# Kernel tuning notes

Measured on AMD Instinct MI355X. Metric: run time of the kernel, lower is better.

The kernel has to match this reference:

```python
import jax, jax.numpy as jnp
import numpy as np

NUM_HEADS = 16


def setup_inputs() -> dict:
    key = jax.random.key(0)
    ks = jax.random.split(key, 10)
    B, S, D = 2, 2048, 1024
    x = jax.random.normal(ks[0], (B, S, D), dtype=jnp.float32)
    mask = jax.random.randint(ks[1], (B, 1, 1, S), 0, 2, dtype=jnp.int32)
    scale = 1.0 / np.sqrt(D)
    wq = jax.random.normal(ks[2], (D, D), dtype=jnp.float32) * scale
    bq = jnp.zeros((D,), dtype=jnp.float32)
    wk = jax.random.normal(ks[3], (D, D), dtype=jnp.float32) * scale
    bk = jnp.zeros((D,), dtype=jnp.float32)
    wv = jax.random.normal(ks[4], (D, D), dtype=jnp.float32) * scale
    bv = jnp.zeros((D,), dtype=jnp.float32)
    wo = jax.random.normal(ks[5], (D, D), dtype=jnp.float32) * scale
    bo = jnp.zeros((D,), dtype=jnp.float32)
    return {"x": x, "mask": mask, "wq": wq, "bq": bq, "wk": wk, "bk": bk,
            "wv": wv, "bv": bv, "wo": wo, "bo": bo}


def reference(x, mask, wq, bq, wk, bk, wv, bv, wo, bo):
    B, S, D = x.shape
    H = NUM_HEADS
    dk = D // H

    def split_heads(t):
        # (B, S, D) -> (B, H, S, dk)
        return t.reshape(B, S, H, dk).transpose(0, 2, 1, 3)

    # PyTorch nn.Linear: y = x @ W^T + b
    q = split_heads(x @ wq.T + bq)
    k = split_heads(x @ wk.T + bk)
    v = split_heads(x @ wv.T + bv)

    # scaled dot-product attention with explicit score matrix (as original)
    logits = jnp.einsum('bhqd,bhkd->bhqk', q, k) / jnp.sqrt(jnp.float32(dk))
    logits = jnp.where(mask == 0, jnp.float32(-1e9), logits)
    attn_weights = jax.nn.softmax(logits, axis=-1)
    # dropout(p=0.1) is identity in eval mode (deterministic reference)
    attn = jnp.einsum('bhqk,bhkd->bhqd', attn_weights, v)

    attn = attn.transpose(0, 2, 1, 3).reshape(B, S, D)
    out = attn @ wo.T + bo
    return out, attn_weights
```

## Files before the change

### kernel.cpp

```cpp
#include <hip/hip_runtime.h>
#include <hip/hip_bf16.h>

#define DEV __device__ __forceinline__

typedef __attribute__((ext_vector_type(8))) __bf16 bf16x8;
typedef __attribute__((ext_vector_type(8))) short s16x8;
typedef __attribute__((ext_vector_type(4))) float f32x4;

DEV f32x4 mfma16(s16x8 a, s16x8 b, f32x4 c){
  return __builtin_amdgcn_mfma_f32_16x16x32_bf16(
      __builtin_bit_cast(bf16x8, a), __builtin_bit_cast(bf16x8, b), c, 0, 0, 0);
}

DEV unsigned short f2bf(float f){
  unsigned int u = __builtin_bit_cast(unsigned int, f);
  u = u + 0x7FFFu + ((u >> 16) & 1u);
  return (unsigned short)(u >> 16);
}

DEV float bf2f(unsigned short u){
  return __builtin_bit_cast(float, ((unsigned int)u) << 16);
}

DEV unsigned long long pack4(float4 v){
  return (unsigned long long)f2bf(v.x) | ((unsigned long long)f2bf(v.y) << 16)
       | ((unsigned long long)f2bf(v.z) << 32) | ((unsigned long long)f2bf(v.w) << 48);
}

DEV unsigned long long pack4f(float a, float b, float c, float d){
  return (unsigned long long)f2bf(a) | ((unsigned long long)f2bf(b) << 16)
       | ((unsigned long long)f2bf(c) << 32) | ((unsigned long long)f2bf(d) << 48);
}

DEV void async16(const void* g, void* l){
  __builtin_amdgcn_global_load_lds(
      (const __attribute__((address_space(1))) unsigned int*)g,
      (__attribute__((address_space(3))) unsigned int*)l, 16, 0, 0);
}

__global__ __launch_bounds__(256) void cvt_kernel(
    const float* __restrict__ x, const float* __restrict__ wq, const float* __restrict__ wk,
    const float* __restrict__ wv, const float* __restrict__ wo,
    const float* __restrict__ bq, const float* __restrict__ bk, const float* __restrict__ bv,
    unsigned long long* __restrict__ xb, unsigned long long* __restrict__ wqkvb,
    unsigned long long* __restrict__ wob, float4* __restrict__ bqkv)
{
  const int i = blockIdx.x * 256 + threadIdx.x;
  const int X4 = 1048576, W4 = 262144;
  if (i < X4){
    xb[i] = pack4(((const float4*)x)[i]);
  } else if (i < X4 + 3*W4){
    int j = i - X4;
    const float* src = (j < W4) ? wq : (j < 2*W4) ? wk : wv;
    int jj = (j < W4) ? j : (j < 2*W4) ? (j - W4) : (j - 2*W4);
    wqkvb[j] = pack4(((const float4*)src)[jj]);
  } else if (i < X4 + 4*W4){
    int j = i - X4 - 3*W4;
    wob[j] = pack4(((const float4*)wo)[j]);
  } else if (i < X4 + 4*W4 + 768){
    int j = i - X4 - 4*W4;
    const float* src = (j < 256) ? bq : (j < 512) ? bk : bv;
    int jj = (j < 256) ? j : (j < 512) ? (j - 256) : (j - 512);
    bqkv[j] = ((const float4*)src)[jj];
  }
}

__global__ __launch_bounds__(256) void gemm_qkv(
    const unsigned short* __restrict__ A,
    const unsigned short* __restrict__ B,
    const float* __restrict__ bias,
    unsigned short* __restrict__ oq,
    unsigned short* __restrict__ okk,
    unsigned short* __restrict__ ovt)
{
  __shared__ __align__(16) char smem[32768];
  char* As = smem;
  char* Bs = smem + 16384;
  const int tid = threadIdx.x;
  const int l = tid & 63, w = tid >> 6, g = l >> 4;

  const int orig = blockIdx.x;
  const int lin = (orig & 7) * 96 + (orig >> 3);
  const int m0 = (lin / 24) * 128, n0 = (lin % 24) * 128;
  const int rowbytes = 2048;

  f32x4 acc[4][4] = {};
  const int wr = w >> 1, wc = w & 1;
  const int wm = wr * 64, wn = wc * 64;

  const int srow = w * 32 + (l >> 3);
  const int scol = (((l & 7) ^ (l >> 3)) << 4);
  const char* Abp = (const char*)A + (size_t)(m0 + srow) * rowbytes + scol;
  const char* Bbp = (const char*)B + (size_t)(n0 + srow) * rowbytes + scol;
  char* Asw = As + w * 4096;
  char* Bsw = Bs + w * 4096;

  int aoff[4][2], boff[4][2];
  for (int mf = 0; mf < 4; ++mf)
    for (int ks = 0; ks < 2; ++ks){
      int ra = wm + mf * 16 + (l & 15);
      aoff[mf][ks] = ra * 128 + ((ks * 64 + g * 16) ^ ((l & 7) << 4));
      int rb = wn + mf * 16 + (l & 15);
      boff[mf][ks] = rb * 128 + ((ks * 64 + g * 16) ^ ((l & 7) << 4));
    }

  for (int kt = 0; kt < 16; ++kt){
    const char* ab = Abp + kt * 128;
    const char* bb = Bbp + kt * 128;
    for (int i = 0; i < 4; ++i){
      async16(ab + (size_t)i * 8 * rowbytes, Asw + i * 1024);
      async16(bb + (size_t)i * 8 * rowbytes, Bsw + i * 1024);
    }
    __syncthreads();
    for (int ks = 0; ks < 2; ++ks){
      s16x8 af[4], bf[4];
      for (int mf = 0; mf < 4; ++mf) af[mf] = *(const s16x8*)(As + aoff[mf][ks]);
      for (int nf = 0; nf < 4; ++nf) bf[nf] = *(const s16x8*)(Bs + boff[nf][ks]);
      for (int mf = 0; mf < 4; ++mf)
        for (int nf = 0; nf < 4; ++nf)
          acc[mf][nf] = mfma16(af[mf], bf[nf], acc[mf][nf]);
    }
    __syncthreads();
  }

  if (n0 >= 2048){
    for (int nf = 0; nf < 4; ++nf){
      int nloc = wn + nf * 16 + (l & 15);
      float bs = bias[n0 + nloc];
      for (int mf = 0; mf < 4; ++mf){
        int mby = (wm + mf * 16 + g * 4) * 2;
        unsigned long long pk = pack4f(acc[mf][nf][0] + bs, acc[mf][nf][1] + bs,
                                       acc[mf][nf][2] + bs, acc[mf][nf][3] + bs);
        *(unsigned long long*)(smem + nloc * 256 + (mby ^ ((nloc & 15) << 4))) = pk;
      }
    }
    __syncthreads();
    int b2 = m0 >> 11, s0 = m0 & 2047;
    for (int i = 0; i < 8; ++i){
      int idx = i * 256 + tid;
      int row = idx >> 4, c8 = (idx & 15) * 8;
      s16x8 vv = *(const s16x8*)(smem + row * 256 + ((c8 * 2) ^ ((row & 15) << 4)));
      *(s16x8*)(ovt + (size_t)(b2 * 1024 + (n0 - 2048) + row) * 2048 + s0 + c8) = vv;
    }
    return;
  }

  for (int mf = 0; mf < 4; ++mf)
    for (int nf = 0; nf < 4; ++nf)
      for (int r = 0; r < 4; ++r){
        int grow = m0 + wm + mf * 16 + g * 4 + r;
        int n = n0 + wn + nf * 16 + (l & 15);
        float v = acc[mf][nf][r] + bias[n];
        if (n < 1024) oq [(size_t)grow * 1024 + n]          = f2bf(v);
        else          okk[(size_t)grow * 1024 + (n - 1024)] = f2bf(v);
      }
}

__global__ __launch_bounds__(256) void gemm_out(
    const unsigned short* __restrict__ A,
    const unsigned short* __restrict__ B,
    const float* __restrict__ bias,
    float* __restrict__ of)
{
  __shared__ __align__(16) char smem[32768];
  char* As = smem;
  char* Bs = smem + 16384;
  const int tid = threadIdx.x, l = tid & 63, w = tid >> 6, g = l >> 4;
  const int orig = blockIdx.x;
  const int lin = (orig & 7) * 64 + (orig >> 3);
  const int m0 = (lin >> 4) * 128, n0 = (lin & 15) * 64;
  const int rowbytes = 2048;

  f32x4 acc[2][4] = {};
  const int wm = w * 32;

  const int scol = (((l & 7) ^ (l >> 3)) << 4);
  const char* Abp = (const char*)A + (size_t)(m0 + w * 32 + (l >> 3)) * rowbytes + scol;
  const char* Bbp = (const char*)B + (size_t)(n0 + w * 16 + (l >> 3)) * rowbytes + scol;
  char* Asw = As + w * 4096;
  char* Bsw = Bs + w * 2048;

  int aoff[2][2], boff[4][2];
  for (int ks = 0; ks < 2; ++ks){
    for (int mf = 0; mf < 2; ++mf){
      int ra = wm + mf * 16 + (l & 15);
      aoff[mf][ks] = ra * 128 + ((ks * 64 + g * 16) ^ ((l & 7) << 4));
    }
    for (int nf = 0; nf < 4; ++nf){
      int rb = nf * 16 + (l & 15);
      boff[nf][ks] = rb * 128 + ((ks * 64 + g * 16) ^ ((l & 7) << 4));
    }
  }

  for (int kt = 0; kt < 16; ++kt){
    for (int i = 0; i < 4; ++i)
      async16(Abp + kt * 128 + (size_t)i * 8 * rowbytes, Asw + i * 1024);
    for (int i = 0; i < 2; ++i)
      async16(Bbp + kt * 128 + (size_t)i * 8 * rowbytes, Bsw + i * 1024);
    __syncthreads();
    for (int ks = 0; ks < 2; ++ks){
      s16x8 af[2], bf[4];
      for (int mf = 0; mf < 2; ++mf) af[mf] = *(const s16x8*)(As + aoff[mf][ks]);
      for (int nf = 0; nf < 4; ++nf) bf[nf] = *(const s16x8*)(Bs + boff[nf][ks]);
      for (int mf = 0; mf < 2; ++mf)
        for (int nf = 0; nf < 4; ++nf)
          acc[mf][nf] = mfma16(af[mf], bf[nf], acc[mf][nf]);
    }
    __syncthreads();
  }

  __syncthreads();
  char* stg = smem + w * 8192;
  float bv4[4];
  for (int nf = 0; nf < 4; ++nf) bv4[nf] = bias[n0 + nf * 16 + (l & 15)];
  for (int mf = 0; mf < 2; ++mf)
    for (int nf = 0; nf < 4; ++nf)
      for (int r = 0; r < 4; ++r){
        int row = mf * 16 + g * 4 + r;
        int colb = (nf * 16 + (l & 15)) * 4;
        *(float*)(stg + row * 256 + (colb ^ ((row & 7) << 4))) = acc[mf][nf][r] + bv4[nf];
      }
  __syncthreads();
  for (int t = 0; t < 8; ++t){
    int row = t * 4 + (l >> 4);
    int colb = ((l & 15) * 16) ^ ((row & 7) << 4);
    f32x4 v = *(const f32x4*)(stg + row * 256 + colb);
    __builtin_nontemporal_store(v, (f32x4*)&of[(size_t)(m0 + wm + row) * 1024 + n0 + (l & 15) * 4]);
  }
}

__global__ __launch_bounds__(256) void attn_kernel(
    const unsigned short* __restrict__ qb,
    const unsigned short* __restrict__ kb,
    const unsigned short* __restrict__ vtb,
    const int* __restrict__ mask,
    float* __restrict__ Pout,
    unsigned short* __restrict__ attnb)
{
  const int flat = blockIdx.x;
  const int sw = (flat & 7) * 256 + (flat >> 3);
  const int qt = sw & 63, h = (sw >> 6) & 15, b = sw >> 10;
  const int tid = threadIdx.x, l = tid & 63, w = tid >> 6, g = l >> 4;
  const int q0 = qt * 32;

  __shared__ float maskadd[2048];
  __shared__ float zpart[4][32];
  __shared__ __align__(16) char est[16384];
  __shared__ __align__(16) float comb[2048];

  for (int i = tid; i < 2048; i += 256)
    maskadd[i] = mask[b * 2048 + i] ? 0.0f : -1e30f;

  s16x8 qf[2][2];
  for (int mf = 0; mf < 2; ++mf)
    for (int ks = 0; ks < 2; ++ks)
      qf[mf][ks] = *(const s16x8*)(qb + (size_t)(b*2048 + q0 + mf*16 + (l&15)) * 1024
                                   + h*64 + ks*32 + g*8);

  const unsigned short* Kb = kb + (size_t)b * 2048 * 1024 + h * 64;
  const unsigned short* Vb = vtb + ((size_t)b * 1024 + h * 64) * 2048;

  __syncthreads();

  float zacc[2] = {0.0f, 0.0f};
  for (int j = 0; j < 8; ++j){
    int kk0 = j * 256 + w * 64;
    f32x4 c[2][4] = {};
    s16x8 kf[4][2];
    for (int nf = 0; nf < 4; ++nf)
      for (int ks = 0; ks < 2; ++ks)
        kf[nf][ks] = *(const s16x8*)(Kb + (size_t)(kk0 + nf*16 + (l&15)) * 1024 + ks*32 + g*8);
    for (int ks = 0; ks < 2; ++ks)
      for (int mf = 0; mf < 2; ++mf)
        for (int nf = 0; nf < 4; ++nf)
          c[mf][nf] = mfma16(kf[nf][ks], qf[mf][ks], c[mf][nf]);
    for (int nf = 0; nf < 4; ++nf){
      f32x4 ma = *(const f32x4*)&maskadd[kk0 + nf*16 + g*4];
      for (int mf = 0; mf < 2; ++mf)
        for (int r = 0; r < 4; ++r)
          zacc[mf] += __expf(fmaf(c[mf][nf][r], 0.125f, ma[r]));
    }
  }
  for (int mf = 0; mf < 2; ++mf){
    float z = zacc[mf];
    z += __shfl_xor(z, 16, 64);
    z += __shfl_xor(z, 32, 64);
    zacc[mf] = z;
  }
  if (g == 0){
    zpart[w][l & 15]        = zacc[0];
    zpart[w][16 + (l & 15)] = zacc[1];
  }
  __syncthreads();
  float zinv[2];
  for (int mf = 0; mf < 2; ++mf){
    int row = mf*16 + (l & 15);
    zinv[mf] = 1.0f / (zpart[0][row] + zpart[1][row] + zpart[2][row] + zpart[3][row]);
  }

  float* Pb = Pout + ((size_t)(b*16 + h) * 2048 + q0) * 2048;
  f32x4 pv[2][4] = {};
  char* estw = est + w * 4096;
  for (int j = 0; j < 8; ++j){
    int kk0 = j * 256 + w * 64;
    f32x4 c[2][4] = {};
    s16x8 kf[4][2];
    for (int nf = 0; nf < 4; ++nf)
      for (int ks = 0; ks < 2; ++ks)
        kf[nf][ks] = *(const s16x8*)(Kb + (size_t)(kk0 + nf*16 + (l&15)) * 1024 + ks*32 + g*8);
    for (int ks = 0; ks < 2; ++ks)
      for (int mf = 0; mf < 2; ++mf)
        for (int nf = 0; nf < 4; ++nf)
          c[mf][nf] = mfma16(kf[nf][ks], qf[mf][ks], c[mf][nf]);
    s16x8 vf[4][2];
    for (int dn = 0; dn < 4; ++dn)
      for (int ks = 0; ks < 2; ++ks)
        vf[dn][ks] = *(const s16x8*)(Vb + (size_t)(dn*16 + (l&15)) * 2048 + kk0 + ks*32 + g*8);
    for (int mf = 0; mf < 2; ++mf){
      int q = mf*16 + (l & 15);
      for (int nf = 0; nf < 4; ++nf){
        f32x4 ma = *(const f32x4*)&maskadd[kk0 + nf*16 + g*4];
        f32x4 p4;
        for (int r = 0; r < 4; ++r)
          p4[r] = __expf(fmaf(c[mf][nf][r], 0.125f, ma[r])) * zinv[mf];
        *(unsigned long long*)(estw + q*128 + ((nf*32 + g*8) ^ ((q & 7) << 4))) =
            pack4f(p4[0], p4[1], p4[2], p4[3]);
      }
    }
    asm volatile("" ::: "memory");
    s16x8 pa[2][2];
    for (int mf = 0; mf < 2; ++mf)
      for (int ks = 0; ks < 2; ++ks){
        int q = mf*16 + (l & 15);
        pa[mf][ks] = *(const s16x8*)(estw + q*128 + ((ks*64 + g*16) ^ ((q & 7) << 4)));
      }
    for (int ks = 0; ks < 2; ++ks)
      for (int mf = 0; mf < 2; ++mf)
        for (int dn = 0; dn < 4; ++dn)
          pv[mf][dn] = mfma16(pa[mf][ks], vf[dn][ks], pv[mf][dn]);
    for (int t = 0; t < 8; ++t){
      int row = t * 4 + (l >> 4);
      unsigned long long pk =
          *(const unsigned long long*)(estw + row*128 + (((l & 15) * 8) ^ ((row & 7) << 4)));
      f32x4 ps;
      ps[0] = bf2f((unsigned short)(pk      ));
      ps[1] = bf2f((unsigned short)(pk >> 16));
      ps[2] = bf2f((unsigned short)(pk >> 32));
      ps[3] = bf2f((unsigned short)(pk >> 48));
      __builtin_nontemporal_store(ps, (f32x4*)&Pb[(size_t)row * 2048 + kk0 + (l & 15) * 4]);
    }
  }

  __syncthreads();
  char* bufw = (w == 0) ? (char*)maskadd : (w == 1) ? est : (w == 2) ? (est + 8192) : (char*)comb;
  for (int mf = 0; mf < 2; ++mf)
    for (int dn = 0; dn < 4; ++dn)
      for (int r = 0; r < 4; ++r){
        int row = mf*16 + g*4 + r, col = dn*16 + (l & 15);
        *(float*)(bufw + row*256 + ((col*4) ^ (((row >> 2) & 3) << 6))) = pv[mf][dn][r];
      }
  __syncthreads();
  {
    int row = tid >> 3, c8 = (tid & 7) * 8;
    int off = row*256 + ((c8*4) ^ (((row >> 2) & 3) << 6));
    f32x4 s0_ = *(f32x4*)((char*)maskadd + off);
    f32x4 s1_ = *(f32x4*)((char*)maskadd + off + 16);
    s0_ += *(f32x4*)(est + off);          s1_ += *(f32x4*)(est + off + 16);
    s0_ += *(f32x4*)(est + 8192 + off);   s1_ += *(f32x4*)(est + 8192 + off + 16);
    s0_ += *(f32x4*)((char*)comb + off);  s1_ += *(f32x4*)((char*)comb + off + 16);
    s16x8 ov;
    for (int t = 0; t < 4; ++t){ ov[t] = (short)f2bf(s0_[t]); ov[t+4] = (short)f2bf(s1_[t]); }
    *(s16x8*)(attnb + (size_t)(b*2048 + q0 + row) * 1024 + h*64 + c8) = ov;
  }
}

extern "C" void kernel_launch(void* const* d_in, const int* in_sizes, int n_in,
                              void* d_out, int out_size, void* d_ws, size_t ws_size,
                              hipStream_t stream)
{
  const float* x  = (const float*)d_in[0];
  const int* mask = (const int*)d_in[1];
  const float* wq = (const float*)d_in[2];
  const float* bq = (const float*)d_in[3];
  const float* wk = (const float*)d_in[4];
  const float* bk = (const float*)d_in[5];
  const float* wv = (const float*)d_in[6];
  const float* bv = (const float*)d_in[7];
  const float* wo = (const float*)d_in[8];
  const float* bo = (const float*)d_in[9];

  char* ws = (char*)d_ws;
  unsigned short* xb    = (unsigned short*)(ws);
  unsigned short* wqkvb = (unsigned short*)(ws + 8388608);
  unsigned short* wob   = (unsigned short*)(ws + 14680064);
  float*          bqkv  = (float*)(ws + 16777216);
  unsigned short* qb    = (unsigned short*)(ws + 16793600);
  unsigned short* kb    = (unsigned short*)(ws + 25182208);
  unsigned short* vtb   = (unsigned short*)(ws + 33570816);
  unsigned short* attnb = (unsigned short*)(ws + 41959424);

  float* fout = (float*)d_out;
  float* Pout = fout + 4194304;

  cvt_kernel<<<8195, 256, 0, stream>>>(x, wq, wk, wv, wo, bq, bk, bv,
                                       (unsigned long long*)xb, (unsigned long long*)wqkvb,
                                       (unsigned long long*)wob, (float4*)bqkv);
  gemm_qkv<<<768, 256, 0, stream>>>(xb, wqkvb, bqkv, qb, kb, vtb);
  attn_kernel<<<2048, 256, 0, stream>>>(qb, kb, vtb, mask, Pout, attnb);
  gemm_out<<<512, 256, 0, stream>>>(attnb, wob, bo, fout);
}
```

Baseline: 281.1 us.

## Cache unnormalized exp scores in LDS to skip recomputing QK^T in second pass

The attention kernel now processes 16 query rows per block instead of 32 and doubles the grid. Each wave owns a contiguous 512-key range. The first pass writes the unnormalized bf16 exp scores into a 64KB LDS buffer, so the second pass no longer reloads K or redoes the QK^T MFMAs and exponentials. Normalization by 1/Z moves to the P store and to the final attention output. The cost is large LDS use per block, which limits occupancy, and halved K/V reuse per block.

After: 321.0 us. 1.14x slower.

```diff
diff --git a/kernel.cpp b/kernel.cpp
--- a/kernel.cpp
+++ b/kernel.cpp
@@ -229,7 +229,7 @@
   }
 }
 
-__global__ __launch_bounds__(256) void attn_kernel(
+__global__ __launch_bounds__(256, 2) void attn_kernel(
     const unsigned short* __restrict__ qb,
     const unsigned short* __restrict__ kb,
     const unsigned short* __restrict__ vtb,
@@ -238,139 +238,108 @@
     unsigned short* __restrict__ attnb)
 {
   const int flat = blockIdx.x;
-  const int sw = (flat & 7) * 256 + (flat >> 3);
-  const int qt = sw & 63, h = (sw >> 6) & 15, b = sw >> 10;
+  const int sw = (flat & 7) * 512 + (flat >> 3);
+  const int qt = sw & 127, h = (sw >> 7) & 15, b = sw >> 11;
   const int tid = threadIdx.x, l = tid & 63, w = tid >> 6, g = l >> 4;
-  const int q0 = qt * 32;
-
+  const int q0 = qt * 16;
+
+  __shared__ __align__(16) char est[65536];
   __shared__ float maskadd[2048];
-  __shared__ float zpart[4][32];
-  __shared__ __align__(16) char est[16384];
-  __shared__ __align__(16) float comb[2048];
+  __shared__ float zpart[4][16];
+  __shared__ float zfullinv[16];
 
   for (int i = tid; i < 2048; i += 256)
     maskadd[i] = mask[b * 2048 + i] ? 0.0f : -1e30f;
 
-  s16x8 qf[2][2];
-  for (int mf = 0; mf < 2; ++mf)
-    for (int ks = 0; ks < 2; ++ks)
-      qf[mf][ks] = *(const s16x8*)(qb + (size_t)(b*2048 + q0 + mf*16 + (l&15)) * 1024
-                                   + h*64 + ks*32 + g*8);
+  s16x8 qf[2];
+  for (int ks = 0; ks < 2; ++ks)
+    qf[ks] = *(const s16x8*)(qb + (size_t)(b*2048 + q0 + (l&15)) * 1024 + h*64 + ks*32 + g*8);
 
   const unsigned short* Kb = kb + (size_t)b * 2048 * 1024 + h * 64;
   const unsigned short* Vb = vtb + ((size_t)b * 1024 + h * 64) * 2048;
 
   __syncthreads();
 
-  float zacc[2] = {0.0f, 0.0f};
+  float zacc = 0.0f;
+  char* estw = est + w * 16384;
+  const int q = l & 15;
   for (int j = 0; j < 8; ++j){
-    int kk0 = j * 256 + w * 64;
-    f32x4 c[2][4] = {};
+    const int kk0 = w * 512 + j * 64;
+    f32x4 c[4] = {};
     s16x8 kf[4][2];
     for (int nf = 0; nf < 4; ++nf)
       for (int ks = 0; ks < 2; ++ks)
         kf[nf][ks] = *(const s16x8*)(Kb + (size_t)(kk0 + nf*16 + (l&15)) * 1024 + ks*32 + g*8);
     for (int ks = 0; ks < 2; ++ks)
-      for (int mf = 0; mf < 2; ++mf)
-        for (int nf = 0; nf < 4; ++nf)
-          c[mf][nf] = mfma16(kf[nf][ks], qf[mf][ks], c[mf][nf]);
+      for (int nf = 0; nf < 4; ++nf)
+        c[nf] = mfma16(kf[nf][ks], qf[ks], c[nf]);
+    char* ej = estw + j * 2048;
     for (int nf = 0; nf < 4; ++nf){
       f32x4 ma = *(const f32x4*)&maskadd[kk0 + nf*16 + g*4];
-      for (int mf = 0; mf < 2; ++mf)
-        for (int r = 0; r < 4; ++r)
-          zacc[mf] += __expf(fmaf(c[mf][nf][r], 0.125f, ma[r]));
-    }
-  }
-  for (int mf = 0; mf < 2; ++mf){
-    float z = zacc[mf];
-    z += __shfl_xor(z, 16, 64);
-    z += __shfl_xor(z, 32, 64);
-    zacc[mf] = z;
-  }
-  if (g == 0){
-    zpart[w][l & 15]        = zacc[0];
-    zpart[w][16 + (l & 15)] = zacc[1];
-  }
-  __syncthreads();
-  float zinv[2];
-  for (int mf = 0; mf < 2; ++mf){
-    int row = mf*16 + (l & 15);
-    zinv[mf] = 1.0f / (zpart[0][row] + zpart[1][row] + zpart[2][row] + zpart[3][row]);
-  }
+      f32x4 e;
+      for (int r = 0; r < 4; ++r){
+        e[r] = __expf(fmaf(c[nf][r], 0.125f, ma[r]));
+        zacc += e[r];
+      }
+      *(unsigned long long*)(ej + q*128 + ((nf*32 + g*8) ^ ((q & 7) << 4))) =
+          pack4f(e[0], e[1], e[2], e[3]);
+    }
+  }
+  zacc += __shfl_xor(zacc, 16, 64);
+  zacc += __shfl_xor(zacc, 32, 64);
+  if (g == 0) zpart[w][q] = zacc;
+  __syncthreads();
+  if (tid < 16)
+    zfullinv[tid] = 1.0f / (zpart[0][tid] + zpart[1][tid] + zpart[2][tid] + zpart[3][tid]);
+  __syncthreads();
 
   float* Pb = Pout + ((size_t)(b*16 + h) * 2048 + q0) * 2048;
-  f32x4 pv[2][4] = {};
-  char* estw = est + w * 4096;
+  f32x4 pv[4] = {};
   for (int j = 0; j < 8; ++j){
-    int kk0 = j * 256 + w * 64;
-    f32x4 c[2][4] = {};
-    s16x8 kf[4][2];
-    for (int nf = 0; nf < 4; ++nf)
-      for (int ks = 0; ks < 2; ++ks)
-        kf[nf][ks] = *(const s16x8*)(Kb + (size_t)(kk0 + nf*16 + (l&15)) * 1024 + ks*32 + g*8);
-    for (int ks = 0; ks < 2; ++ks)
-      for (int mf = 0; mf < 2; ++mf)
-        for (int nf = 0; nf < 4; ++nf)
-          c[mf][nf] = mfma16(kf[nf][ks], qf[mf][ks], c[mf][nf]);
+    const int kk0 = w * 512 + j * 64;
+    char* ej = estw + j * 2048;
     s16x8 vf[4][2];
     for (int dn = 0; dn < 4; ++dn)
       for (int ks = 0; ks < 2; ++ks)
         vf[dn][ks] = *(const s16x8*)(Vb + (size_t)(dn*16 + (l&15)) * 2048 + kk0 + ks*32 + g*8);
-    for (int mf = 0; mf < 2; ++mf){
-      int q = mf*16 + (l & 15);
-      for (int nf = 0; nf < 4; ++nf){
-        f32x4 ma = *(const f32x4*)&maskadd[kk0 + nf*16 + g*4];
-        f32x4 p4;
-        for (int r = 0; r < 4; ++r)
-          p4[r] = __expf(fmaf(c[mf][nf][r], 0.125f, ma[r])) * zinv[mf];
-        *(unsigned long long*)(estw + q*128 + ((nf*32 + g*8) ^ ((q & 7) << 4))) =
-            pack4f(p4[0], p4[1], p4[2], p4[3]);
-      }
-    }
-    asm volatile("" ::: "memory");
-    s16x8 pa[2][2];
-    for (int mf = 0; mf < 2; ++mf)
-      for (int ks = 0; ks < 2; ++ks){
-        int q = mf*16 + (l & 15);
-        pa[mf][ks] = *(const s16x8*)(estw + q*128 + ((ks*64 + g*16) ^ ((q & 7) << 4)));
-      }
+    s16x8 pa[2];
     for (int ks = 0; ks < 2; ++ks)
-      for (int mf = 0; mf < 2; ++mf)
-        for (int dn = 0; dn < 4; ++dn)
-          pv[mf][dn] = mfma16(pa[mf][ks], vf[dn][ks], pv[mf][dn]);
-    for (int t = 0; t < 8; ++t){
-      int row = t * 4 + (l >> 4);
+      pa[ks] = *(const s16x8*)(ej + q*128 + ((ks*64 + g*16) ^ ((q & 7) << 4)));
+    for (int ks = 0; ks < 2; ++ks)
+      for (int dn = 0; dn < 4; ++dn)
+        pv[dn] = mfma16(pa[ks], vf[dn][ks], pv[dn]);
+    for (int t = 0; t < 4; ++t){
+      int row = t * 4 + g;
       unsigned long long pk =
-          *(const unsigned long long*)(estw + row*128 + (((l & 15) * 8) ^ ((row & 7) << 4)));
+          *(const unsigned long long*)(ej + row*128 + (((l & 15) * 8) ^ ((row & 7) << 4)));
+      float zr = zfullinv[row];
       f32x4 ps;
-      ps[0] = bf2f((unsigned short)(pk      ));
-      ps[1] = bf2f((unsigned short)(pk >> 16));
-      ps[2] = bf2f((unsigned short)(pk >> 32));
-      ps[3] = bf2f((unsigned short)(pk >> 48));
+      ps[0] = bf2f((unsigned short)(pk      )) * zr;
+      ps[1] = bf2f((unsigned short)(pk >> 16)) * zr;
+      ps[2] = bf2f((unsigned short)(pk >> 32)) * zr;
+      ps[3] = bf2f((unsigned short)(pk >> 48)) * zr;
       __builtin_nontemporal_store(ps, (f32x4*)&Pb[(size_t)row * 2048 + kk0 + (l & 15) * 4]);
     }
   }
 
   __syncthreads();
-  char* bufw = (w == 0) ? (char*)maskadd : (w == 1) ? est : (w == 2) ? (est + 8192) : (char*)comb;
-  for (int mf = 0; mf < 2; ++mf)
-    for (int dn = 0; dn < 4; ++dn)
-      for (int r = 0; r < 4; ++r){
-        int row = mf*16 + g*4 + r, col = dn*16 + (l & 15);
-        *(float*)(bufw + row*256 + ((col*4) ^ (((row >> 2) & 3) << 6))) = pv[mf][dn][r];
-      }
+  char* bufw = est + w * 4096;
+  for (int dn = 0; dn < 4; ++dn)
+    for (int r = 0; r < 4; ++r){
+      int row = g*4 + r, col = dn*16 + (l & 15);
+      *(float*)(bufw + row*256 + ((col*4) ^ (((row >> 2) & 3) << 6))) = pv[dn][r];
+    }
   __syncthreads();
   {
-    int row = tid >> 3, c8 = (tid & 7) * 8;
-    int off = row*256 + ((c8*4) ^ (((row >> 2) & 3) << 6));
-    f32x4 s0_ = *(f32x4*)((char*)maskadd + off);
-    f32x4 s1_ = *(f32x4*)((char*)maskadd + off + 16);
-    s0_ += *(f32x4*)(est + off);          s1_ += *(f32x4*)(est + off + 16);
-    s0_ += *(f32x4*)(est + 8192 + off);   s1_ += *(f32x4*)(est + 8192 + off + 16);
-    s0_ += *(f32x4*)((char*)comb + off);  s1_ += *(f32x4*)((char*)comb + off + 16);
-    s16x8 ov;
-    for (int t = 0; t < 4; ++t){ ov[t] = (short)f2bf(s0_[t]); ov[t+4] = (short)f2bf(s1_[t]); }
-    *(s16x8*)(attnb + (size_t)(b*2048 + q0 + row) * 1024 + h*64 + c8) = ov;
+    int row = tid >> 4;
+    int off = row*256 + (((tid & 15) * 16) ^ (((row >> 2) & 3) << 6));
+    f32x4 s = *(const f32x4*)(est + off);
+    s += *(const f32x4*)(est + 4096 + off);
+    s += *(const f32x4*)(est + 8192 + off);
+    s += *(const f32x4*)(est + 12288 + off);
+    float zr = zfullinv[row];
+    unsigned long long ov = pack4f(s[0]*zr, s[1]*zr, s[2]*zr, s[3]*zr);
+    *(unsigned long long*)&attnb[(size_t)(b*2048 + q0 + row) * 1024 + h*64 + (tid & 15) * 4] = ov;
   }
 }
 
@@ -406,6 +375,6 @@
                                        (unsigned long long*)xb, (unsigned long long*)wqkvb,
                                        (unsigned long long*)wob, (float4*)bqkv);
   gemm_qkv<<<768, 256, 0, stream>>>(xb, wqkvb, bqkv, qb, kb, vtb);
-  attn_kernel<<<2048, 256, 0, stream>>>(qb, kb, vtb, mask, Pout, attnb);
+  attn_kernel<<<4096, 256, 0, stream>>>(qb, kb, vtb, mask, Pout, attnb);
   gemm_out<<<512, 256, 0, stream>>>(attnb, wob, bo, fout);
 }
```
